# Kernel tuning notes

Hardware: AMD Instinct MI355X
Metric: run time of the kernel (lower is better)

Reference implementation:

```python
import jax, jax.numpy as jnp
import numpy as np

N_NODES = 50000


def gcn_conv(x, W, src, dst, n):
    # PyG GCNConv(bias=False): h = x @ W, then symmetric-normalized
    # aggregation over A + I (self-loops added, normalize=True).
    h = x @ W  # [N, F_out]
    loop = jnp.arange(n, dtype=src.dtype)
    s = jnp.concatenate([src, loop])  # source nodes (messages come from x_j = h[s])
    d = jnp.concatenate([dst, loop])  # target nodes (aggregation index)
    ones = jnp.ones(s.shape[0], dtype=h.dtype)
    deg = jax.ops.segment_sum(ones, d, num_segments=n)  # in-degree incl. self-loop
    dinv = jnp.where(deg > 0, jax.lax.rsqrt(deg), 0.0)
    norm = dinv[s] * dinv[d]  # per-edge D^-1/2 A_hat D^-1/2 weight
    msgs = h[s] * norm[:, None]  # gather + scale
    return jax.ops.segment_sum(msgs, d, num_segments=n)  # scatter-add


def setup_inputs() -> dict:
    key = jax.random.key(0)
    k1, k2, k3, k4 = jax.random.split(key, 4)
    x = jax.random.normal(k1, (N_NODES, 256), dtype=jnp.float32)
    edge_index = jax.random.randint(k2, (2, 1600000), 0, N_NODES, dtype=jnp.int64)
    # glorot-scale weights
    W1 = jax.random.normal(k3, (256, 256), dtype=jnp.float32) * (1.0 / np.sqrt(256))
    W3 = jax.random.normal(k4, (256, 64), dtype=jnp.float32) * (1.0 / np.sqrt(256))
    return {"x": x, "edge_index": edge_index, "W1": W1, "W3": W3}


def reference(x, edge_index, W1, W3):
    n = x.shape[0]
    src, dst = edge_index[0], edge_index[1]
    h = jax.nn.relu(gcn_conv(x, W1, src, dst, n))
    h = jax.nn.relu(gcn_conv(h, W3, src, dst, n))
    return h
```

## Files before the change

### kernel.cpp

```cpp
#include <hip/hip_runtime.h>
#include <cstdint>
#include <cstddef>


#define NPART 128

__device__ __forceinline__ float bf2f(unsigned short u) {
    union { unsigned int i; float f; } c; c.i = ((unsigned int)u) << 16; return c.f;
}
__device__ __forceinline__ unsigned short f2bf(float f) {
    union { float f; unsigned int i; } c; c.f = f;
    unsigned int r = c.i + 0x7fffu + ((c.i >> 16) & 1u);
    return (unsigned short)(r >> 16);
}


__global__ __launch_bounds__(256) void cvt_f32_bf16(const float* __restrict__ in,
                                                    unsigned short* __restrict__ out,
                                                    int nElem8) {
    int i = blockIdx.x * blockDim.x + threadIdx.x;
    if (i < nElem8) {
        const float4 a = *(const float4*)(in + (size_t)i * 8);
        const float4 b = *(const float4*)(in + (size_t)i * 8 + 4);
        union { unsigned short u[8]; uint4 v; } pk;
        pk.u[0] = f2bf(a.x); pk.u[1] = f2bf(a.y); pk.u[2] = f2bf(a.z); pk.u[3] = f2bf(a.w);
        pk.u[4] = f2bf(b.x); pk.u[5] = f2bf(b.y); pk.u[6] = f2bf(b.z); pk.u[7] = f2bf(b.w);
        *(uint4*)(out + (size_t)i * 8) = pk.v;
    }
}

__global__ __launch_bounds__(256) void wcvt_kernel(const float* __restrict__ W,
                                                   unsigned short* __restrict__ Wt,
                                                   int K, int N) {
    int idx = blockIdx.x * blockDim.x + threadIdx.x;
    if (idx < N * K) {
        int nn = idx / K, kk = idx % K;
        Wt[idx] = f2bf(W[(size_t)kk * N + nn]);
    }
}


__global__ __launch_bounds__(256) void part_hist(const int* __restrict__ dst, int E, int NB,
                                                 int* __restrict__ blockhist) {
    __shared__ int lh[1024];
    for (int t = threadIdx.x; t < NB; t += 256) lh[t] = 0;
    __syncthreads();
    const int per = (E + NPART - 1) / NPART;
    const int beg = blockIdx.x * per;
    const int end = min(E, beg + per);
    for (int i = beg + threadIdx.x; i < end; i += 256)
        atomicAdd(&lh[dst[i] >> 6], 1);
    __syncthreads();
    for (int t = threadIdx.x; t < NB; t += 256)
        blockhist[blockIdx.x * NB + t] = lh[t];
}

__global__ __launch_bounds__(1024) void part_scan(const int* __restrict__ blockhist,
                                                  int* __restrict__ bofs,
                                                  int* __restrict__ bbase, int NB) {
    __shared__ int wsum[16];
    const int t = threadIdx.x;
    const int lane = t & 63;
    int tot = 0;
    if (t < NB)
        for (int k = 0; k < NPART; ++k) tot += blockhist[k * NB + t];
    int x = tot;
    #pragma unroll
    for (int off = 1; off < 64; off <<= 1) {
        int q = __shfl_up(x, off);
        if (lane >= off) x += q;
    }
    if (lane == 63) wsum[t >> 6] = x;
    __syncthreads();
    if (t < 64) {
        int y = (t < 16) ? wsum[t] : 0;
        #pragma unroll
        for (int off = 1; off < 16; off <<= 1) {
            int q = __shfl_up(y, off);
            if (lane >= off) y += q;
        }
        if (t < 16) wsum[t] = y;
    }
    __syncthreads();
    int excl = ((t >> 6) ? wsum[(t >> 6) - 1] : 0) + x - tot;
    if (t < NB) {
        bofs[t] = excl;
        if (t == NB - 1) bofs[NB] = excl + tot;
        int run = excl;
        for (int k = 0; k < NPART; ++k) {
            int c = blockhist[k * NB + t];
            bbase[k * NB + t] = run;
            run += c;
        }
    }
}

__global__ __launch_bounds__(256) void part_scatter(const int* __restrict__ src,
                                                    const int* __restrict__ dst,
                                                    const int* __restrict__ bbase,
                                                    uint2* __restrict__ pairs, int E, int NB) {
    __shared__ int lbase[1024];
    for (int t = threadIdx.x; t < NB; t += 256) lbase[t] = bbase[blockIdx.x * NB + t];
    __syncthreads();
    const int per = (E + NPART - 1) / NPART;
    const int beg = blockIdx.x * per;
    const int end = min(E, beg + per);
    for (int i = beg + threadIdx.x; i < end; i += 256) {
        int d = dst[i];
        int off = atomicAdd(&lbase[d >> 6], 1);
        pairs[off] = make_uint2((unsigned)src[i], (unsigned)d);
    }
}

__global__ __launch_bounds__(256) void bucket_build(const uint2* __restrict__ pairs,
                                                    const int* __restrict__ bofs,
                                                    int* __restrict__ rowptr,
                                                    float* __restrict__ dinv,
                                                    int* __restrict__ csr, int n) {
    const int b = blockIdx.x;
    const int node0 = b << 6;
    __shared__ int ldeg[64], lcur[64];
    if (threadIdx.x < 64) ldeg[threadIdx.x] = 0;
    __syncthreads();
    const int beg = bofs[b], end = bofs[b + 1];
    for (int i = beg + threadIdx.x; i < end; i += 256)
        atomicAdd(&ldeg[pairs[i].y & 63], 1);
    __syncthreads();
    if (threadIdx.x < 64) {
        const int lane = threadIdx.x;
        int v = ldeg[lane];
        int x = v;
        #pragma unroll
        for (int off = 1; off < 64; off <<= 1) {
            int q = __shfl_up(x, off);
            if (lane >= off) x += q;
        }
        int excl = x - v;
        int node = node0 + lane;
        if (node < n) {
            rowptr[node] = beg + excl;
            dinv[node] = rsqrtf((float)(v + 1));
        }
        lcur[lane] = beg + excl;
        if (b == (int)gridDim.x - 1 && lane == 0) rowptr[n] = end;
    }
    __syncthreads();
    for (int i = beg + threadIdx.x; i < end; i += 256) {
        uint2 p = pairs[i];
        int pos = atomicAdd(&lcur[p.y & 63], 1);
        csr[pos] = (int)p.x;
    }
}

template<int BN, int WM, int WN>
__global__ __launch_bounds__(256) void mfma_gemm(const unsigned short* __restrict__ Ab,
                                                 const unsigned short* __restrict__ Bt,
                                                 unsigned short* __restrict__ C,
                                                 int M, int N, int K) {
    constexpr int BM = 128, BK = 64;
    constexpr int KP = 72;
    constexpr int WTM = BM / WM;
    constexpr int WTN = BN / WN;
    constexpr int MF = WTM / 16;
    constexpr int NF = WTN / 16;
    __shared__ unsigned short As[BM][KP];
    __shared__ unsigned short Bs[BN][KP];
    const int tid = threadIdx.x;
    const int wid = tid >> 6;
    const int lane = tid & 63;
    const int wr = wid / WN;
    const int wc = wid % WN;
    const int bm = blockIdx.y * BM;
    const int bn = blockIdx.x * BN;
    const int l15 = lane & 15;
    const int lg = lane >> 4;

    using bf16x8 = __attribute__((ext_vector_type(8))) short;
    using f32x4  = __attribute__((ext_vector_type(4))) float;
    f32x4 acc[MF][NF] = {};

    for (int k0 = 0; k0 < K; k0 += BK) {
        #pragma unroll
        for (int it = 0; it < (BM * BK / 8) / 256; ++it) {
            int v = tid + 256 * it;
            int row = v >> 3;
            int oct = v & 7;
            uint4 val = make_uint4(0, 0, 0, 0);
            int gr = bm + row;
            if (gr < M) val = *(const uint4*)(Ab + (size_t)gr * K + k0 + oct * 8);
            *(uint4*)(&As[row][oct * 8]) = val;
        }
        #pragma unroll
        for (int it = 0; it < (BN * BK / 8) / 256; ++it) {
            int v = tid + 256 * it;
            int row = v >> 3;
            int oct = v & 7;
            uint4 val = *(const uint4*)(Bt + (size_t)(bn + row) * K + k0 + oct * 8);
            *(uint4*)(&Bs[row][oct * 8]) = val;
        }
        __syncthreads();
        bf16x8 af[MF][2], bfr[NF][2];
        #pragma unroll
        for (int m = 0; m < MF; ++m)
            #pragma unroll
            for (int kk = 0; kk < 2; ++kk)
                af[m][kk] = *(const bf16x8*)(&As[wr * WTM + m * 16 + l15][kk * 32 + lg * 8]);
        #pragma unroll
        for (int nf = 0; nf < NF; ++nf)
            #pragma unroll
            for (int kk = 0; kk < 2; ++kk)
                bfr[nf][kk] = *(const bf16x8*)(&Bs[wc * WTN + nf * 16 + l15][kk * 32 + lg * 8]);
        #pragma unroll
        for (int kk = 0; kk < 2; ++kk)
            #pragma unroll
            for (int m = 0; m < MF; ++m)
                #pragma unroll
                for (int nf = 0; nf < NF; ++nf)
                    acc[m][nf] = __builtin_amdgcn_mfma_f32_16x16x32_bf16(
                        af[m][kk], bfr[nf][kk], acc[m][nf], 0, 0, 0);
        __syncthreads();
    }
    #pragma unroll
    for (int m = 0; m < MF; ++m) {
        #pragma unroll
        for (int j = 0; j < 4; ++j) {
            int row = bm + wr * WTM + m * 16 + lg * 4 + j;
            if (row < M) {
                #pragma unroll
                for (int nf = 0; nf < NF; ++nf) {
                    int col = bn + wc * WTN + nf * 16 + l15;
                    C[(size_t)row * N + col] = f2bf(acc[m][nf][j]);
                }
            }
        }
    }
}


__global__ __launch_bounds__(256) void aggregate256_kernel(
        const unsigned short* __restrict__ h, const int* __restrict__ rowptr,
        const int* __restrict__ csr_src, const float* __restrict__ dinv,
        unsigned short* __restrict__ out, int n) {
    const int d = blockIdx.x;
    const int tid = threadIdx.x;
    const int wid = tid >> 6;
    const int lane = tid & 63;
    const float wd = dinv[d];
    const int beg = rowptr[d];
    const int end = rowptr[d + 1];

    float acc0 = 0.f, acc1 = 0.f, acc2 = 0.f, acc3 = 0.f;
    if (wid == 0) {
        ushort4 t = *(const ushort4*)(h + (size_t)d * 256 + lane * 4);
        float w2 = wd * wd;
        acc0 = bf2f(t.x) * w2; acc1 = bf2f(t.y) * w2;
        acc2 = bf2f(t.z) * w2; acc3 = bf2f(t.w) * w2;
    }

    __shared__ int   ssrc[256];
    __shared__ float sw[256];
    for (int k0 = beg; k0 < end; k0 += 256) {
        int cnt = min(256, end - k0);
        if (tid < cnt) {
            int s = csr_src[k0 + tid];
            ssrc[tid] = s;
            sw[tid] = dinv[s] * wd;
        }
        __syncthreads();
        #pragma unroll 4
        for (int e = wid; e < cnt; e += 4) {
            ushort4 t = *(const ushort4*)(h + (size_t)ssrc[e] * 256 + lane * 4);
            float w = sw[e];
            acc0 = fmaf(bf2f(t.x), w, acc0);
            acc1 = fmaf(bf2f(t.y), w, acc1);
            acc2 = fmaf(bf2f(t.z), w, acc2);
            acc3 = fmaf(bf2f(t.w), w, acc3);
        }
        __syncthreads();
    }

    __shared__ float part[3][256];
    if (wid > 0) {
        part[wid - 1][lane * 4 + 0] = acc0;
        part[wid - 1][lane * 4 + 1] = acc1;
        part[wid - 1][lane * 4 + 2] = acc2;
        part[wid - 1][lane * 4 + 3] = acc3;
    }
    __syncthreads();
    if (wid == 0) {
        acc0 += part[0][lane*4+0] + part[1][lane*4+0] + part[2][lane*4+0];
        acc1 += part[0][lane*4+1] + part[1][lane*4+1] + part[2][lane*4+1];
        acc2 += part[0][lane*4+2] + part[1][lane*4+2] + part[2][lane*4+2];
        acc3 += part[0][lane*4+3] + part[1][lane*4+3] + part[2][lane*4+3];
        union { unsigned short u[4]; uint2 v; } pk;
        pk.u[0] = f2bf(fmaxf(acc0, 0.f));
        pk.u[1] = f2bf(fmaxf(acc1, 0.f));
        pk.u[2] = f2bf(fmaxf(acc2, 0.f));
        pk.u[3] = f2bf(fmaxf(acc3, 0.f));
        *(uint2*)(out + (size_t)d * 256 + lane * 4) = pk.v;
    }
}

__global__ __launch_bounds__(256) void aggregate64_kernel(
        const unsigned short* __restrict__ h, const int* __restrict__ rowptr,
        const int* __restrict__ csr_src, const float* __restrict__ dinv,
        float* __restrict__ out, int n) {
    const int d = blockIdx.x;
    const int tid = threadIdx.x;
    const int wid = tid >> 6;
    const int lane = tid & 63;
    const float wd = dinv[d];
    const int beg = rowptr[d];
    const int end = rowptr[d + 1];

    float acc = 0.f;
    if (wid == 0) acc = bf2f(h[(size_t)d * 64 + lane]) * wd * wd;

    __shared__ int   ssrc[256];
    __shared__ float sw[256];
    for (int k0 = beg; k0 < end; k0 += 256) {
        int cnt = min(256, end - k0);
        if (tid < cnt) {
            int s = csr_src[k0 + tid];
            ssrc[tid] = s;
            sw[tid] = dinv[s] * wd;
        }
        __syncthreads();
        #pragma unroll 4
        for (int e = wid; e < cnt; e += 4) {
            acc = fmaf(bf2f(h[(size_t)ssrc[e] * 64 + lane]), sw[e], acc);
        }
        __syncthreads();
    }

    __shared__ float part[3][64];
    if (wid > 0) part[wid - 1][lane] = acc;
    __syncthreads();
    if (wid == 0) {
        acc += part[0][lane] + part[1][lane] + part[2][lane];
        out[(size_t)d * 64 + lane] = fmaxf(acc, 0.f);
    }
}


static inline size_t align256(size_t v) { return (v + 255) & ~(size_t)255; }

extern "C" void kernel_launch(void* const* d_in, const int* in_sizes, int n_in,
                              void* d_out, int out_size, void* d_ws, size_t ws_size,
                              hipStream_t stream) {
    const float* x  = (const float*)d_in[0];
    const int*   ei = (const int*)d_in[1];
    const float* W1 = (const float*)d_in[2];
    const float* W3 = (const float*)d_in[3];

    const int n = in_sizes[0] / 256;
    const int E = in_sizes[1] / 2;
    const int NB = (n + 63) >> 6;
    const int* src = ei;
    const int* dst = ei + E;

    char* w = (char*)d_ws;
    auto alloc = [&](size_t bytes) { char* p = w; w += align256(bytes); return p; };
    unsigned short* xb   = (unsigned short*)alloc((size_t)n * 256 * 2);
    unsigned short* h1   = (unsigned short*)alloc((size_t)n * 256 * 2);
    unsigned short* a1   = (unsigned short*)alloc((size_t)n * 256 * 2);
    unsigned short* h2   = (unsigned short*)alloc((size_t)n * 64 * 2);
    unsigned short* W1t  = (unsigned short*)alloc(256 * 256 * 2);
    unsigned short* W3t  = (unsigned short*)alloc(64 * 256 * 2);
    float* dinv          = (float*)alloc((size_t)n * 4);
    int*   rowptr        = (int*)alloc((size_t)(n + 1) * 4);
    int*   csr           = (int*)alloc((size_t)E * 4);
    uint2* pairs         = (uint2*)alloc((size_t)E * 8);
    int*   blockhist     = (int*)alloc((size_t)NPART * NB * 4);
    int*   bbase         = (int*)alloc((size_t)NPART * NB * 4);
    int*   bofs          = (int*)alloc((size_t)(NB + 1) * 4);
    float* out           = (float*)d_out;

    cvt_f32_bf16<<<((n * 256 / 8) + 255) / 256, 256, 0, stream>>>(x, xb, n * 256 / 8);
    wcvt_kernel<<<(256 * 256 + 255) / 256, 256, 0, stream>>>(W1, W1t, 256, 256);
    wcvt_kernel<<<(64 * 256 + 255) / 256, 256, 0, stream>>>(W3, W3t, 256, 64);

    part_hist<<<NPART, 256, 0, stream>>>(dst, E, NB, blockhist);
    part_scan<<<1, 1024, 0, stream>>>(blockhist, bofs, bbase, NB);
    part_scatter<<<NPART, 256, 0, stream>>>(src, dst, bbase, pairs, E, NB);
    bucket_build<<<NB, 256, 0, stream>>>(pairs, bofs, rowptr, dinv, csr, n);

    {
        dim3 grid(256 / 128, (n + 127) / 128);
        mfma_gemm<128, 2, 2><<<grid, 256, 0, stream>>>(xb, W1t, h1, n, 256, 256);
        aggregate256_kernel<<<n, 256, 0, stream>>>(h1, rowptr, csr, dinv, a1, n);
    }
    {
        dim3 grid(1, (n + 127) / 128);
        mfma_gemm<64, 4, 1><<<grid, 256, 0, stream>>>(a1, W3t, h2, n, 64, 256);
        aggregate64_kernel<<<n, 256, 0, stream>>>(h2, rowptr, csr, dinv, out, n);
    }
}
```

Measured before the change: 300.2 us.

## Tile aggregation by column slices per XCD, fuse x conversion into GEMM, precompute edge weights

Replaces the one-block-per-node aggregation with kernels where each 32-lane group handles one node and a 32-column slice. Block indices are mapped so each XCD works on one column tile, which is meant to keep its slice of h resident in that XCD's L2. A new pass packs each CSR source index with its dinv into a uint2, so the shared-memory staging and its barriers are no longer needed. The separate f32-to-bf16 conversion of x is folded into the first GEMM's A load. The risks are uncoalesced 64-byte gathers per edge, the extra epair_fill pass over all edges, and that the L2 locality depends on how the hardware assigns blocks to XCDs.

Measured after the change: 421.9 us. 40.5% more time.

```diff
diff --git a/kernel.cpp b/kernel.cpp
--- a/kernel.cpp
+++ b/kernel.cpp
@@ -12,21 +12,6 @@
     union { float f; unsigned int i; } c; c.f = f;
     unsigned int r = c.i + 0x7fffu + ((c.i >> 16) & 1u);
     return (unsigned short)(r >> 16);
-}
-
-
-__global__ __launch_bounds__(256) void cvt_f32_bf16(const float* __restrict__ in,
-                                                    unsigned short* __restrict__ out,
-                                                    int nElem8) {
-    int i = blockIdx.x * blockDim.x + threadIdx.x;
-    if (i < nElem8) {
-        const float4 a = *(const float4*)(in + (size_t)i * 8);
-        const float4 b = *(const float4*)(in + (size_t)i * 8 + 4);
-        union { unsigned short u[8]; uint4 v; } pk;
-        pk.u[0] = f2bf(a.x); pk.u[1] = f2bf(a.y); pk.u[2] = f2bf(a.z); pk.u[3] = f2bf(a.w);
-        pk.u[4] = f2bf(b.x); pk.u[5] = f2bf(b.y); pk.u[6] = f2bf(b.z); pk.u[7] = f2bf(b.w);
-        *(uint4*)(out + (size_t)i * 8) = pk.v;
-    }
 }
 
 __global__ __launch_bounds__(256) void wcvt_kernel(const float* __restrict__ W,
@@ -62,8 +47,10 @@
     const int t = threadIdx.x;
     const int lane = t & 63;
     int tot = 0;
-    if (t < NB)
+    if (t < NB) {
+        #pragma unroll 4
         for (int k = 0; k < NPART; ++k) tot += blockhist[k * NB + t];
+    }
     int x = tot;
     #pragma unroll
     for (int off = 1; off < 64; off <<= 1) {
@@ -152,8 +139,18 @@
     }
 }
 
-template<int BN, int WM, int WN>
-__global__ __launch_bounds__(256) void mfma_gemm(const unsigned short* __restrict__ Ab,
+__global__ __launch_bounds__(256) void epair_fill(const int* __restrict__ csr,
+                                                  const float* __restrict__ dinv,
+                                                  uint2* __restrict__ ep, int E) {
+    int i = blockIdx.x * blockDim.x + threadIdx.x;
+    if (i < E) {
+        int s = csr[i];
+        ep[i] = make_uint2((unsigned)s, __float_as_uint(dinv[s]));
+    }
+}
+
+template<int BN, int WM, int WN, bool AF32>
+__global__ __launch_bounds__(256) void mfma_gemm(const void* __restrict__ Av,
                                                  const unsigned short* __restrict__ Bt,
                                                  unsigned short* __restrict__ C,
                                                  int M, int N, int K) {
@@ -187,7 +184,22 @@
             int oct = v & 7;
             uint4 val = make_uint4(0, 0, 0, 0);
             int gr = bm + row;
-            if (gr < M) val = *(const uint4*)(Ab + (size_t)gr * K + k0 + oct * 8);
+            if (gr < M) {
+                if (AF32) {
+                    const float* A32 = (const float*)Av;
+                    float4 f0 = *(const float4*)(A32 + (size_t)gr * K + k0 + oct * 8);
+                    float4 f1 = *(const float4*)(A32 + (size_t)gr * K + k0 + oct * 8 + 4);
+                    union { unsigned short u[8]; uint4 v4; } pk;
+                    pk.u[0] = f2bf(f0.x); pk.u[1] = f2bf(f0.y);
+                    pk.u[2] = f2bf(f0.z); pk.u[3] = f2bf(f0.w);
+                    pk.u[4] = f2bf(f1.x); pk.u[5] = f2bf(f1.y);
+                    pk.u[6] = f2bf(f1.z); pk.u[7] = f2bf(f1.w);
+                    val = pk.v4;
+                } else {
+                    const unsigned short* Ab = (const unsigned short*)Av;
+                    val = *(const uint4*)(Ab + (size_t)gr * K + k0 + oct * 8);
+                }
+            }
             *(uint4*)(&As[row][oct * 8]) = val;
         }
         #pragma unroll
@@ -236,110 +248,73 @@
     }
 }
 
-
-__global__ __launch_bounds__(256) void aggregate256_kernel(
+__global__ __launch_bounds__(256) void agg256_tiled(
         const unsigned short* __restrict__ h, const int* __restrict__ rowptr,
-        const int* __restrict__ csr_src, const float* __restrict__ dinv,
+        const uint2* __restrict__ ep, const float* __restrict__ dinv,
         unsigned short* __restrict__ out, int n) {
-    const int d = blockIdx.x;
-    const int tid = threadIdx.x;
-    const int wid = tid >> 6;
-    const int lane = tid & 63;
+    const int b = blockIdx.x;
+    const int tile = b & 7;
+    const int nb = b >> 3;
+    const int hw = threadIdx.x >> 5;
+    const int c  = threadIdx.x & 31;
+    const int d  = nb * 8 + hw;
+    if (d >= n) return;
+    const int col = tile * 32 + c;
     const float wd = dinv[d];
-    const int beg = rowptr[d];
-    const int end = rowptr[d + 1];
-
-    float acc0 = 0.f, acc1 = 0.f, acc2 = 0.f, acc3 = 0.f;
-    if (wid == 0) {
-        ushort4 t = *(const ushort4*)(h + (size_t)d * 256 + lane * 4);
-        float w2 = wd * wd;
-        acc0 = bf2f(t.x) * w2; acc1 = bf2f(t.y) * w2;
-        acc2 = bf2f(t.z) * w2; acc3 = bf2f(t.w) * w2;
-    }
-
-    __shared__ int   ssrc[256];
-    __shared__ float sw[256];
-    for (int k0 = beg; k0 < end; k0 += 256) {
-        int cnt = min(256, end - k0);
-        if (tid < cnt) {
-            int s = csr_src[k0 + tid];
-            ssrc[tid] = s;
-            sw[tid] = dinv[s] * wd;
-        }
-        __syncthreads();
-        #pragma unroll 4
-        for (int e = wid; e < cnt; e += 4) {
-            ushort4 t = *(const ushort4*)(h + (size_t)ssrc[e] * 256 + lane * 4);
-            float w = sw[e];
-            acc0 = fmaf(bf2f(t.x), w, acc0);
-            acc1 = fmaf(bf2f(t.y), w, acc1);
-            acc2 = fmaf(bf2f(t.z), w, acc2);
-            acc3 = fmaf(bf2f(t.w), w, acc3);
-        }
-        __syncthreads();
-    }
-
-    __shared__ float part[3][256];
-    if (wid > 0) {
-        part[wid - 1][lane * 4 + 0] = acc0;
-        part[wid - 1][lane * 4 + 1] = acc1;
-        part[wid - 1][lane * 4 + 2] = acc2;
-        part[wid - 1][lane * 4 + 3] = acc3;
-    }
-    __syncthreads();
-    if (wid == 0) {
-        acc0 += part[0][lane*4+0] + part[1][lane*4+0] + part[2][lane*4+0];
-        acc1 += part[0][lane*4+1] + part[1][lane*4+1] + part[2][lane*4+1];
-        acc2 += part[0][lane*4+2] + part[1][lane*4+2] + part[2][lane*4+2];
-        acc3 += part[0][lane*4+3] + part[1][lane*4+3] + part[2][lane*4+3];
-        union { unsigned short u[4]; uint2 v; } pk;
-        pk.u[0] = f2bf(fmaxf(acc0, 0.f));
-        pk.u[1] = f2bf(fmaxf(acc1, 0.f));
-        pk.u[2] = f2bf(fmaxf(acc2, 0.f));
-        pk.u[3] = f2bf(fmaxf(acc3, 0.f));
-        *(uint2*)(out + (size_t)d * 256 + lane * 4) = pk.v;
-    }
-}
-
-__global__ __launch_bounds__(256) void aggregate64_kernel(
+    float acc = bf2f(h[(size_t)d * 256 + col]) * wd * wd;
+    const int beg = rowptr[d], end = rowptr[d + 1];
+    int k = beg;
+    for (; k + 4 <= end; k += 4) {
+        uint2 e0 = ep[k], e1 = ep[k + 1], e2 = ep[k + 2], e3 = ep[k + 3];
+        float v0 = bf2f(h[(size_t)e0.x * 256 + col]);
+        float v1 = bf2f(h[(size_t)e1.x * 256 + col]);
+        float v2 = bf2f(h[(size_t)e2.x * 256 + col]);
+        float v3 = bf2f(h[(size_t)e3.x * 256 + col]);
+        acc = fmaf(v0, __uint_as_float(e0.y) * wd, acc);
+        acc = fmaf(v1, __uint_as_float(e1.y) * wd, acc);
+        acc = fmaf(v2, __uint_as_float(e2.y) * wd, acc);
+        acc = fmaf(v3, __uint_as_float(e3.y) * wd, acc);
+    }
+    for (; k < end; ++k) {
+        uint2 e = ep[k];
+        acc = fmaf(bf2f(h[(size_t)e.x * 256 + col]), __uint_as_float(e.y) * wd, acc);
+    }
+    out[(size_t)d * 256 + col] = f2bf(fmaxf(acc, 0.f));
+}
+
+__global__ __launch_bounds__(256) void agg64_tiled(
         const unsigned short* __restrict__ h, const int* __restrict__ rowptr,
-        const int* __restrict__ csr_src, const float* __restrict__ dinv,
+        const uint2* __restrict__ ep, const float* __restrict__ dinv,
         float* __restrict__ out, int n) {
-    const int d = blockIdx.x;
-    const int tid = threadIdx.x;
-    const int wid = tid >> 6;
-    const int lane = tid & 63;
+    const int b = blockIdx.x;
+    const int xcd = b & 7;
+    const int tile = xcd >> 2;
+    const int nb = (b >> 3) * 4 + (xcd & 3);
+    const int hw = threadIdx.x >> 5;
+    const int c  = threadIdx.x & 31;
+    const int d  = nb * 8 + hw;
+    if (d >= n) return;
+    const int col = tile * 32 + c;
     const float wd = dinv[d];
-    const int beg = rowptr[d];
-    const int end = rowptr[d + 1];
-
-    float acc = 0.f;
-    if (wid == 0) acc = bf2f(h[(size_t)d * 64 + lane]) * wd * wd;
-
-    __shared__ int   ssrc[256];
-    __shared__ float sw[256];
-    for (int k0 = beg; k0 < end; k0 += 256) {
-        int cnt = min(256, end - k0);
-        if (tid < cnt) {
-            int s = csr_src[k0 + tid];
-            ssrc[tid] = s;
-            sw[tid] = dinv[s] * wd;
-        }
-        __syncthreads();
-        #pragma unroll 4
-        for (int e = wid; e < cnt; e += 4) {
-            acc = fmaf(bf2f(h[(size_t)ssrc[e] * 64 + lane]), sw[e], acc);
-        }
-        __syncthreads();
-    }
-
-    __shared__ float part[3][64];
-    if (wid > 0) part[wid - 1][lane] = acc;
-    __syncthreads();
-    if (wid == 0) {
-        acc += part[0][lane] + part[1][lane] + part[2][lane];
-        out[(size_t)d * 64 + lane] = fmaxf(acc, 0.f);
-    }
+    float acc = bf2f(h[(size_t)d * 64 + col]) * wd * wd;
+    const int beg = rowptr[d], end = rowptr[d + 1];
+    int k = beg;
+    for (; k + 4 <= end; k += 4) {
+        uint2 e0 = ep[k], e1 = ep[k + 1], e2 = ep[k + 2], e3 = ep[k + 3];
+        float v0 = bf2f(h[(size_t)e0.x * 64 + col]);
+        float v1 = bf2f(h[(size_t)e1.x * 64 + col]);
+        float v2 = bf2f(h[(size_t)e2.x * 64 + col]);
+        float v3 = bf2f(h[(size_t)e3.x * 64 + col]);
+        acc = fmaf(v0, __uint_as_float(e0.y) * wd, acc);
+        acc = fmaf(v1, __uint_as_float(e1.y) * wd, acc);
+        acc = fmaf(v2, __uint_as_float(e2.y) * wd, acc);
+        acc = fmaf(v3, __uint_as_float(e3.y) * wd, acc);
+    }
+    for (; k < end; ++k) {
+        uint2 e = ep[k];
+        acc = fmaf(bf2f(h[(size_t)e.x * 64 + col]), __uint_as_float(e.y) * wd, acc);
+    }
+    out[(size_t)d * 64 + col] = fmaxf(acc, 0.f);
 }
 
 
@@ -361,7 +336,6 @@
 
     char* w = (char*)d_ws;
     auto alloc = [&](size_t bytes) { char* p = w; w += align256(bytes); return p; };
-    unsigned short* xb   = (unsigned short*)alloc((size_t)n * 256 * 2);
     unsigned short* h1   = (unsigned short*)alloc((size_t)n * 256 * 2);
     unsigned short* a1   = (unsigned short*)alloc((size_t)n * 256 * 2);
     unsigned short* h2   = (unsigned short*)alloc((size_t)n * 64 * 2);
@@ -371,12 +345,12 @@
     int*   rowptr        = (int*)alloc((size_t)(n + 1) * 4);
     int*   csr           = (int*)alloc((size_t)E * 4);
     uint2* pairs         = (uint2*)alloc((size_t)E * 8);
+    uint2* epairs        = (uint2*)alloc((size_t)E * 8);
     int*   blockhist     = (int*)alloc((size_t)NPART * NB * 4);
     int*   bbase         = (int*)alloc((size_t)NPART * NB * 4);
     int*   bofs          = (int*)alloc((size_t)(NB + 1) * 4);
     float* out           = (float*)d_out;
 
-    cvt_f32_bf16<<<((n * 256 / 8) + 255) / 256, 256, 0, stream>>>(x, xb, n * 256 / 8);
     wcvt_kernel<<<(256 * 256 + 255) / 256, 256, 0, stream>>>(W1, W1t, 256, 256);
     wcvt_kernel<<<(64 * 256 + 255) / 256, 256, 0, stream>>>(W3, W3t, 256, 64);
 
@@ -384,15 +358,19 @@
     part_scan<<<1, 1024, 0, stream>>>(blockhist, bofs, bbase, NB);
     part_scatter<<<NPART, 256, 0, stream>>>(src, dst, bbase, pairs, E, NB);
     bucket_build<<<NB, 256, 0, stream>>>(pairs, bofs, rowptr, dinv, csr, n);
+    epair_fill<<<(E + 255) / 256, 256, 0, stream>>>(csr, dinv, epairs, E);
 
     {
         dim3 grid(256 / 128, (n + 127) / 128);
-        mfma_gemm<128, 2, 2><<<grid, 256, 0, stream>>>(xb, W1t, h1, n, 256, 256);
-        aggregate256_kernel<<<n, 256, 0, stream>>>(h1, rowptr, csr, dinv, a1, n);
+        mfma_gemm<128, 2, 2, true><<<grid, 256, 0, stream>>>(x, W1t, h1, n, 256, 256);
+        int nb8 = (n + 7) / 8;
+        agg256_tiled<<<nb8 * 8, 256, 0, stream>>>(h1, rowptr, epairs, dinv, a1, n);
     }
     {
         dim3 grid(1, (n + 127) / 128);
-        mfma_gemm<64, 4, 1><<<grid, 256, 0, stream>>>(a1, W3t, h2, n, 64, 256);
-        aggregate64_kernel<<<n, 256, 0, stream>>>(h2, rowptr, csr, dinv, out, n);
-    }
-}
+        mfma_gemm<64, 4, 1, false><<<grid, 256, 0, stream>>>(a1, W3t, h2, n, 64, 256);
+        int nb8 = (n + 7) / 8;
+        int q = (nb8 + 3) / 4;
+        agg64_tiled<<<q * 8, 256, 0, stream>>>(h2, rowptr, epairs, dinv, out, n);
+    }
+}
```

## Fuse x conversion into GEMM, sort CSR by source chunk, precompute edge offsets

Applied to the files above, without the earlier changes.

Removes the standalone f32-to-bf16 conversion of x by converting inside the first GEMM's A-tile load. bucket_build now orders each node's neighbour list by source chunk (src>>12), which should make gathers more cache-local. A new epair_fill kernel precomputes byte offsets and dinv per edge, so the aggregation kernels do one coalesced 8-byte load per edge instead of an index load plus a dependent dinv gather. It also raises the unroll factors. The cost is an extra kernel launch, an extra E*8 buffer, and a larger shared histogram.

Result: slower. 316.0 us (+5.3%).

```diff
diff --git a/kernel.cpp b/kernel.cpp
--- a/kernel.cpp
+++ b/kernel.cpp
@@ -4,6 +4,8 @@
 
 
 #define NPART 128
+#define NCHUNK 16
+#define CHUNK_SHIFT 12
 
 __device__ __forceinline__ float bf2f(unsigned short u) {
     union { unsigned int i; float f; } c; c.i = ((unsigned int)u) << 16; return c.f;
@@ -12,21 +14,6 @@
     union { float f; unsigned int i; } c; c.f = f;
     unsigned int r = c.i + 0x7fffu + ((c.i >> 16) & 1u);
     return (unsigned short)(r >> 16);
-}
-
-
-__global__ __launch_bounds__(256) void cvt_f32_bf16(const float* __restrict__ in,
-                                                    unsigned short* __restrict__ out,
-                                                    int nElem8) {
-    int i = blockIdx.x * blockDim.x + threadIdx.x;
-    if (i < nElem8) {
-        const float4 a = *(const float4*)(in + (size_t)i * 8);
-        const float4 b = *(const float4*)(in + (size_t)i * 8 + 4);
-        union { unsigned short u[8]; uint4 v; } pk;
-        pk.u[0] = f2bf(a.x); pk.u[1] = f2bf(a.y); pk.u[2] = f2bf(a.z); pk.u[3] = f2bf(a.w);
-        pk.u[4] = f2bf(b.x); pk.u[5] = f2bf(b.y); pk.u[6] = f2bf(b.z); pk.u[7] = f2bf(b.w);
-        *(uint4*)(out + (size_t)i * 8) = pk.v;
-    }
 }
 
 __global__ __launch_bounds__(256) void wcvt_kernel(const float* __restrict__ W,
@@ -62,8 +49,10 @@
     const int t = threadIdx.x;
     const int lane = t & 63;
     int tot = 0;
-    if (t < NB)
+    if (t < NB) {
+        #pragma unroll 4
         for (int k = 0; k < NPART; ++k) tot += blockhist[k * NB + t];
+    }
     int x = tot;
     #pragma unroll
     for (int off = 1; off < 64; off <<= 1) {
@@ -119,41 +108,69 @@
                                                     int* __restrict__ csr, int n) {
     const int b = blockIdx.x;
     const int node0 = b << 6;
-    __shared__ int ldeg[64], lcur[64];
-    if (threadIdx.x < 64) ldeg[threadIdx.x] = 0;
+    __shared__ int hist[64 * NCHUNK];
+    for (int t = threadIdx.x; t < 64 * NCHUNK; t += 256) hist[t] = 0;
     __syncthreads();
     const int beg = bofs[b], end = bofs[b + 1];
-    for (int i = beg + threadIdx.x; i < end; i += 256)
-        atomicAdd(&ldeg[pairs[i].y & 63], 1);
-    __syncthreads();
-    if (threadIdx.x < 64) {
-        const int lane = threadIdx.x;
-        int v = ldeg[lane];
-        int x = v;
-        #pragma unroll
-        for (int off = 1; off < 64; off <<= 1) {
-            int q = __shfl_up(x, off);
-            if (lane >= off) x += q;
-        }
-        int excl = x - v;
-        int node = node0 + lane;
-        if (node < n) {
-            rowptr[node] = beg + excl;
-            dinv[node] = rsqrtf((float)(v + 1));
-        }
-        lcur[lane] = beg + excl;
-        if (b == (int)gridDim.x - 1 && lane == 0) rowptr[n] = end;
-    }
-    __syncthreads();
+    const int cnt = end - beg;
     for (int i = beg + threadIdx.x; i < end; i += 256) {
         uint2 p = pairs[i];
-        int pos = atomicAdd(&lcur[p.y & 63], 1);
-        csr[pos] = (int)p.x;
-    }
-}
-
-template<int BN, int WM, int WN>
-__global__ __launch_bounds__(256) void mfma_gemm(const unsigned short* __restrict__ Ab,
+        atomicAdd(&hist[(p.y & 63) * NCHUNK + (p.x >> CHUNK_SHIFT)], 1);
+    }
+    __syncthreads();
+    const int base = threadIdx.x * 4;
+    int s0 = hist[base], s1 = hist[base + 1], s2 = hist[base + 2], s3 = hist[base + 3];
+    int tsum = s0 + s1 + s2 + s3;
+    const int lane = threadIdx.x & 63;
+    const int wid = threadIdx.x >> 6;
+    int x = tsum;
+    #pragma unroll
+    for (int off = 1; off < 64; off <<= 1) {
+        int q = __shfl_up(x, off);
+        if (lane >= off) x += q;
+    }
+    __shared__ int wsum[4];
+    if (lane == 63) wsum[wid] = x;
+    __syncthreads();
+    int woff = 0;
+    #pragma unroll
+    for (int k = 0; k < 4; ++k) if (k < wid) woff += wsum[k];
+    int excl = woff + x - tsum;
+    hist[base]     = excl;
+    hist[base + 1] = excl + s0;
+    hist[base + 2] = excl + s0 + s1;
+    hist[base + 3] = excl + s0 + s1 + s2;
+    __syncthreads();
+    if (threadIdx.x < 64) {
+        int start = hist[threadIdx.x * NCHUNK];
+        int next  = (threadIdx.x == 63) ? cnt : hist[(threadIdx.x + 1) * NCHUNK];
+        int node = node0 + threadIdx.x;
+        if (node < n) {
+            rowptr[node] = beg + start;
+            dinv[node] = rsqrtf((float)(next - start + 1));
+        }
+    }
+    if (b == (int)gridDim.x - 1 && threadIdx.x == 0) rowptr[n] = end;
+    __syncthreads();
+    for (int i = beg + threadIdx.x; i < end; i += 256) {
+        uint2 p = pairs[i];
+        int pos = atomicAdd(&hist[(p.y & 63) * NCHUNK + (p.x >> CHUNK_SHIFT)], 1);
+        csr[beg + pos] = (int)p.x;
+    }
+}
+
+__global__ __launch_bounds__(256) void epair_fill(const int* __restrict__ csr,
+                                                  const float* __restrict__ dinv,
+                                                  uint2* __restrict__ ep, int E) {
+    int i = blockIdx.x * blockDim.x + threadIdx.x;
+    if (i < E) {
+        int s = csr[i];
+        ep[i] = make_uint2((unsigned)s * 512u, __float_as_uint(dinv[s]));
+    }
+}
+
+template<int BN, int WM, int WN, bool AF32>
+__global__ __launch_bounds__(256) void mfma_gemm(const void* __restrict__ Av,
                                                  const unsigned short* __restrict__ Bt,
                                                  unsigned short* __restrict__ C,
                                                  int M, int N, int K) {
@@ -187,7 +204,22 @@
             int oct = v & 7;
             uint4 val = make_uint4(0, 0, 0, 0);
             int gr = bm + row;
-            if (gr < M) val = *(const uint4*)(Ab + (size_t)gr * K + k0 + oct * 8);
+            if (gr < M) {
+                if (AF32) {
+                    const float* A32 = (const float*)Av;
+                    float4 f0 = *(const float4*)(A32 + (size_t)gr * K + k0 + oct * 8);
+                    float4 f1 = *(const float4*)(A32 + (size_t)gr * K + k0 + oct * 8 + 4);
+                    union { unsigned short u[8]; uint4 v4; } pk;
+                    pk.u[0] = f2bf(f0.x); pk.u[1] = f2bf(f0.y);
+                    pk.u[2] = f2bf(f0.z); pk.u[3] = f2bf(f0.w);
+                    pk.u[4] = f2bf(f1.x); pk.u[5] = f2bf(f1.y);
+                    pk.u[6] = f2bf(f1.z); pk.u[7] = f2bf(f1.w);
+                    val = pk.v4;
+                } else {
+                    const unsigned short* Ab = (const unsigned short*)Av;
+                    val = *(const uint4*)(Ab + (size_t)gr * K + k0 + oct * 8);
+                }
+            }
             *(uint4*)(&As[row][oct * 8]) = val;
         }
         #pragma unroll
@@ -236,10 +268,9 @@
     }
 }
 
-
 __global__ __launch_bounds__(256) void aggregate256_kernel(
         const unsigned short* __restrict__ h, const int* __restrict__ rowptr,
-        const int* __restrict__ csr_src, const float* __restrict__ dinv,
+        const uint2* __restrict__ ep, const float* __restrict__ dinv,
         unsigned short* __restrict__ out, int n) {
     const int d = blockIdx.x;
     const int tid = threadIdx.x;
@@ -257,19 +288,20 @@
         acc2 = bf2f(t.z) * w2; acc3 = bf2f(t.w) * w2;
     }
 
-    __shared__ int   ssrc[256];
+    __shared__ unsigned int soff[256];
     __shared__ float sw[256];
+    const char* hb = (const char*)h;
     for (int k0 = beg; k0 < end; k0 += 256) {
         int cnt = min(256, end - k0);
         if (tid < cnt) {
-            int s = csr_src[k0 + tid];
-            ssrc[tid] = s;
-            sw[tid] = dinv[s] * wd;
-        }
-        __syncthreads();
-        #pragma unroll 4
+            uint2 p = ep[k0 + tid];
+            soff[tid] = p.x;
+            sw[tid] = __uint_as_float(p.y) * wd;
+        }
+        __syncthreads();
+        #pragma unroll 8
         for (int e = wid; e < cnt; e += 4) {
-            ushort4 t = *(const ushort4*)(h + (size_t)ssrc[e] * 256 + lane * 4);
+            ushort4 t = *(const ushort4*)(hb + soff[e] + lane * 8);
             float w = sw[e];
             acc0 = fmaf(bf2f(t.x), w, acc0);
             acc1 = fmaf(bf2f(t.y), w, acc1);
@@ -303,7 +335,7 @@
 
 __global__ __launch_bounds__(256) void aggregate64_kernel(
         const unsigned short* __restrict__ h, const int* __restrict__ rowptr,
-        const int* __restrict__ csr_src, const float* __restrict__ dinv,
+        const uint2* __restrict__ ep, const float* __restrict__ dinv,
         float* __restrict__ out, int n) {
     const int d = blockIdx.x;
     const int tid = threadIdx.x;
@@ -316,19 +348,21 @@
     float acc = 0.f;
     if (wid == 0) acc = bf2f(h[(size_t)d * 64 + lane]) * wd * wd;
 
-    __shared__ int   ssrc[256];
+    __shared__ unsigned int soff[256];
     __shared__ float sw[256];
+    const char* hb = (const char*)h;
     for (int k0 = beg; k0 < end; k0 += 256) {
         int cnt = min(256, end - k0);
         if (tid < cnt) {
-            int s = csr_src[k0 + tid];
-            ssrc[tid] = s;
-            sw[tid] = dinv[s] * wd;
-        }
-        __syncthreads();
-        #pragma unroll 4
+            uint2 p = ep[k0 + tid];
+            soff[tid] = p.x >> 2;
+            sw[tid] = __uint_as_float(p.y) * wd;
+        }
+        __syncthreads();
+        #pragma unroll 8
         for (int e = wid; e < cnt; e += 4) {
-            acc = fmaf(bf2f(h[(size_t)ssrc[e] * 64 + lane]), sw[e], acc);
+            unsigned short t = *(const unsigned short*)(hb + soff[e] + lane * 2);
+            acc = fmaf(bf2f(t), sw[e], acc);
         }
         __syncthreads();
     }
@@ -361,7 +395,6 @@
 
     char* w = (char*)d_ws;
     auto alloc = [&](size_t bytes) { char* p = w; w += align256(bytes); return p; };
-    unsigned short* xb   = (unsigned short*)alloc((size_t)n * 256 * 2);
     unsigned short* h1   = (unsigned short*)alloc((size_t)n * 256 * 2);
     unsigned short* a1   = (unsigned short*)alloc((size_t)n * 256 * 2);
     unsigned short* h2   = (unsigned short*)alloc((size_t)n * 64 * 2);
@@ -371,12 +404,12 @@
     int*   rowptr        = (int*)alloc((size_t)(n + 1) * 4);
     int*   csr           = (int*)alloc((size_t)E * 4);
     uint2* pairs         = (uint2*)alloc((size_t)E * 8);
+    uint2* epairs        = (uint2*)alloc((size_t)E * 8);
     int*   blockhist     = (int*)alloc((size_t)NPART * NB * 4);
     int*   bbase         = (int*)alloc((size_t)NPART * NB * 4);
     int*   bofs          = (int*)alloc((size_t)(NB + 1) * 4);
     float* out           = (float*)d_out;
 
-    cvt_f32_bf16<<<((n * 256 / 8) + 255) / 256, 256, 0, stream>>>(x, xb, n * 256 / 8);
     wcvt_kernel<<<(256 * 256 + 255) / 256, 256, 0, stream>>>(W1, W1t, 256, 256);
     wcvt_kernel<<<(64 * 256 + 255) / 256, 256, 0, stream>>>(W3, W3t, 256, 64);
 
@@ -384,15 +417,16 @@
     part_scan<<<1, 1024, 0, stream>>>(blockhist, bofs, bbase, NB);
     part_scatter<<<NPART, 256, 0, stream>>>(src, dst, bbase, pairs, E, NB);
     bucket_build<<<NB, 256, 0, stream>>>(pairs, bofs, rowptr, dinv, csr, n);
+    epair_fill<<<(E + 255) / 256, 256, 0, stream>>>(csr, dinv, epairs, E);
 
     {
         dim3 grid(256 / 128, (n + 127) / 128);
-        mfma_gemm<128, 2, 2><<<grid, 256, 0, stream>>>(xb, W1t, h1, n, 256, 256);
-        aggregate256_kernel<<<n, 256, 0, stream>>>(h1, rowptr, csr, dinv, a1, n);
+        mfma_gemm<128, 2, 2, true><<<grid, 256, 0, stream>>>(x, W1t, h1, n, 256, 256);
+        aggregate256_kernel<<<n, 256, 0, stream>>>(h1, rowptr, epairs, dinv, a1, n);
     }
     {
         dim3 grid(1, (n + 127) / 128);
-        mfma_gemm<64, 4, 1><<<grid, 256, 0, stream>>>(a1, W3t, h2, n, 64, 256);
-        aggregate64_kernel<<<n, 256, 0, stream>>>(h2, rowptr, csr, dinv, out, n);
-    }
-}
+        mfma_gemm<64, 4, 1, false><<<grid, 256, 0, stream>>>(a1, W3t, h2, n, 64, 256);
+        aggregate64_kernel<<<n, 256, 0, stream>>>(h2, rowptr, epairs, dinv, out, n);
+    }
+}
```
